# Optimization experiments

Hardware: AMD Instinct MI355X
Metric: run time of the kernel (lower is better)

Reference implementation:

```python
import jax, jax.numpy as jnp
import numpy as np
from jax import lax

D_MODEL = 512
N_STATE = 64
L = 1024
NC = 4  # n_components
HIDDEN = 2 * D_MODEL  # ChannelMix mult=2
R = D_MODEL // 8      # SE reduction
EPS = 1e-5


def hippo_A(N):
    n = np.arange(N, dtype=np.float32)
    t = 2.0 * n + 1.0
    sq = np.sqrt(t[:, None] * t[None, :])
    A = -np.tril(sq, -1) - np.diag(n + 1.0)
    return jnp.asarray(A, jnp.float32)


def setup_inputs() -> dict:
    key = jax.random.key(0)
    ks = jax.random.split(key, 12)
    d, N = D_MODEL, N_STATE
    n = np.arange(N, dtype=np.float32)
    Bref = jnp.asarray(np.sqrt(2.0 * n + 1.0), jnp.float32)
    Bp = jnp.tile(Bref[None, None, :], (NC, d, 1)) + 0.01 * jax.random.normal(ks[0], (NC, d, N))
    Cp = 0.1 * jax.random.normal(ks[1], (NC, d, N))
    Dp = jnp.zeros((NC, d))
    log_dt = jnp.log(0.1 * (1.5 ** jnp.arange(NC, dtype=jnp.float32)))
    x = jax.random.normal(ks[2], (8, L, d))
    s = 0.02
    return {
        "x": x,
        "Bp": Bp, "Cp": Cp, "Dp": Dp, "log_dt": log_dt,
        "se_w1": s * jax.random.normal(ks[3], (R, d)), "se_b1": jnp.zeros((R,)),
        "se_w2": s * jax.random.normal(ks[4], (d, R)), "se_b2": jnp.zeros((d,)),
        "n1_g": jnp.ones((d,)), "n1_b": jnp.zeros((d,)),
        "up_w": s * jax.random.normal(ks[5], (2 * HIDDEN, d)), "up_b": jnp.zeros((2 * HIDDEN,)),
        "down_w": s * jax.random.normal(ks[6], (d, HIDDEN)), "down_b": jnp.zeros((d,)),
        "mixn_g": jnp.ones((d,)), "mixn_b": jnp.zeros((d,)),
        "n2_g": jnp.ones((d,)), "n2_b": jnp.zeros((d,)),
    }


def _ln(x, g, b):
    m = jnp.mean(x, axis=-1, keepdims=True)
    v = jnp.mean(jnp.square(x - m), axis=-1, keepdims=True)
    return (x - m) * lax.rsqrt(v + EPS) * g + b


def _mixture_kernel(Bp, Cp, Dp, log_dt):
    A = hippo_A(N_STATE)
    I = jnp.eye(N_STATE, dtype=jnp.float32)

    def one(Bc, Cc, Dc, ldt):
        dt = jax.nn.softplus(ldt) + 1e-6
        lhs = I - 0.5 * dt * A
        rhs = I + 0.5 * dt * A
        A_bar = jnp.linalg.solve(lhs, rhs)          # (N,N)
        B_bar = jnp.linalg.solve(lhs, (dt * Bc).T).T  # (d,N)

        def step(xs, _):
            y = jnp.einsum('dn,dn->d', Cc, xs)
            return xs @ A_bar.T, y

        _, ys = lax.scan(step, B_bar, None, length=L)  # (L,d)
        K = ys.T  # (d,L)
        return K.at[:, 0].add(Dc)

    return jax.vmap(one)(Bp, Cp, Dp, log_dt).sum(0)  # (d,L)


def reference(x, Bp, Cp, Dp, log_dt,
              se_w1, se_b1, se_w2, se_b2,
              n1_g, n1_b, up_w, up_b, down_w, down_b,
              mixn_g, mixn_b, n2_g, n2_b):
    d = D_MODEL
    K = _mixture_kernel(Bp, Cp, Dp, log_dt)  # (d,L)

    # causal full-length depthwise conv1d
    x_dw = jnp.transpose(x, (0, 2, 1))  # (B,C,T)
    x_pad = jnp.pad(x_dw, ((0, 0), (0, 0), (L - 1, 0)))
    y = lax.conv_general_dilated(
        x_pad, K[:, None, :], window_strides=(1,), padding='VALID',
        feature_group_count=d, dimension_numbers=('NCH', 'OIH', 'NCH'))
    y = jnp.transpose(y, (0, 2, 1))  # (B,T,C)

    # SE gate (squeeze over time)
    s = jnp.mean(y, axis=1)  # (B,C)
    h = jax.nn.relu(s @ se_w1.T + se_b1)
    g = jax.nn.sigmoid(h @ se_w2.T + se_b2)
    y = y * g[:, None, :]

    y1 = _ln(x + y, n1_g, n1_b)

    # ChannelMix (GLU MLP) with residual + LN
    u = y1 @ up_w.T + up_b
    a, gg = jnp.split(u, 2, axis=-1)
    z = (jax.nn.gelu(a, approximate=False) * jax.nn.sigmoid(gg)) @ down_w.T + down_b
    z = _ln(y1 + z, mixn_g, mixn_b)

    return _ln(y1 + z, n2_g, n2_b)
```

## Files before the change

kernel.cpp:

```cpp
#include <hip/hip_runtime.h>
#include <math.h>


typedef short bf16x8 __attribute__((ext_vector_type(8)));
typedef float f32x4 __attribute__((ext_vector_type(4)));

__device__ __forceinline__ float fast_sigmoid(float x) { return 1.0f / (1.0f + __expf(-x)); }
__device__ __forceinline__ float fast_gelu(float x) {
    float u = 0.7978845608f * (x + 0.044715f * x * x * x);
    float t = 1.0f - 2.0f / (1.0f + __expf(2.0f * u));
    return 0.5f * x * (1.0f + t);
}
__device__ __forceinline__ unsigned short f2bf(float f) {
    unsigned u = __float_as_uint(f);
    unsigned r = (u + 0x7FFFu + ((u >> 16) & 1u)) >> 16;
    return (unsigned short)r;
}
__device__ __forceinline__ unsigned pk2(unsigned short a, unsigned short b) {
    return (unsigned)a | ((unsigned)b << 16);
}
__device__ __forceinline__ void gload16(const void* g, void* l) {
    __builtin_amdgcn_global_load_lds((const __attribute__((address_space(1))) unsigned int*)g,
                                     (__attribute__((address_space(3))) unsigned int*)l, 16, 0, 0);
}

__global__ __launch_bounds__(256) void front_kernel(const float* __restrict__ log_dt,
                                                    const float* __restrict__ Bp,
                                                    const float* __restrict__ up_w,
                                                    const float* __restrict__ dn_w,
                                                    const float* __restrict__ Cp,
                                                    const float* __restrict__ x,
                                                    float* __restrict__ Pow,
                                                    unsigned short* __restrict__ Bb_h,
                                                    unsigned short* __restrict__ Bb_l,
                                                    unsigned short* __restrict__ up_wb,
                                                    unsigned short* __restrict__ dn_wb,
                                                    unsigned short* __restrict__ Cp_h,
                                                    unsigned short* __restrict__ Cp_l,
                                                    float* __restrict__ xT) {
    __shared__ __align__(16) float smem[16640];
    int bid = blockIdx.x, tid = threadIdx.x;
    if (bid < 4) {
        float* M1 = smem;
        float* M1T = smem + 4096;
        float* M2 = smem + 8192;
        float* M2T = smem + 12288;
        int comp = bid;
        float ldt = log_dt[comp];
        float dt = log1pf(expf(ldt)) + 1e-6f;
        float hdt = 0.5f * dt;
        if (tid < 64) {
            int j = tid;
            float sqj = sqrtf(2.0f * (float)j + 1.0f);
            float S = 0.0f;
            for (int i = 0; i < 64; ++i) {
                float sqi = sqrtf(2.0f * (float)i + 1.0f);
                float r = (i == j) ? (1.0f - hdt * (float)(i + 1))
                                   : ((i > j) ? (-hdt * sqi * sqj) : 0.0f);
                float X = (r - hdt * sqi * S) / (1.0f + hdt * (float)(i + 1));
                M1[i * 64 + j] = X;
                M1T[j * 64 + i] = X;
                S += sqi * X;
            }
        }
        __syncthreads();
        for (int ii = tid; ii < 4096; ii += 256) Pow[(size_t)comp * 40960 + ii] = M1[ii];
        float* cur = M1; float* curT = M1T; float* nxt = M2; float* nxtT = M2T;
        int ti = tid >> 4, tj = tid & 15;
        for (int s = 1; s <= 9; ++s) {
            float c[4][4] = {{0}};
#pragma unroll 8
            for (int k = 0; k < 64; ++k) {
                float4 a = *(const float4*)&curT[k * 64 + ti * 4];
                float4 b = *(const float4*)&cur[k * 64 + tj * 4];
                c[0][0] += a.x * b.x; c[0][1] += a.x * b.y; c[0][2] += a.x * b.z; c[0][3] += a.x * b.w;
                c[1][0] += a.y * b.x; c[1][1] += a.y * b.y; c[1][2] += a.y * b.z; c[1][3] += a.y * b.w;
                c[2][0] += a.z * b.x; c[2][1] += a.z * b.y; c[2][2] += a.z * b.z; c[2][3] += a.z * b.w;
                c[3][0] += a.w * b.x; c[3][1] += a.w * b.y; c[3][2] += a.w * b.z; c[3][3] += a.w * b.w;
            }
#pragma unroll
            for (int r = 0; r < 4; ++r) {
                float4 row; row.x = c[r][0]; row.y = c[r][1]; row.z = c[r][2]; row.w = c[r][3];
                *(float4*)&nxt[(ti * 4 + r) * 64 + tj * 4] = row;
                float4 colv; colv.x = c[0][r]; colv.y = c[1][r]; colv.z = c[2][r]; colv.w = c[3][r];
                *(float4*)&nxtT[(tj * 4 + r) * 64 + ti * 4] = colv;
            }
            __syncthreads();
            for (int ii = tid; ii < 4096; ii += 256) Pow[(size_t)comp * 40960 + s * 4096 + ii] = nxt[ii];
            float* t0 = cur; cur = nxt; nxt = t0;
            float* t1 = curT; curT = nxtT; nxtT = t1;
            __syncthreads();
        }
    } else if (bid < 12) {
        int gid = (bid - 4) * 256 + tid;
        int comp = gid >> 9;
        float ldt = log_dt[comp];
        float dt = log1pf(expf(ldt)) + 1e-6f;
        float hdt = 0.5f * dt;
        const float* bp = Bp + (size_t)gid * 64;
        unsigned short* oh = Bb_h + (size_t)gid * 64;
        unsigned short* ol = Bb_l + (size_t)gid * 64;
        float S = 0.0f;
        for (int i = 0; i < 64; ++i) {
            float sqi = sqrtf(2.0f * (float)i + 1.0f);
            float y = (dt * bp[i] - hdt * sqi * S) / (1.0f + hdt * (float)(i + 1));
            unsigned short h = f2bf(y);
            oh[i] = h;
            ol[i] = f2bf(y - __uint_as_float((unsigned)h << 16));
            S += sqi * y;
        }
    } else if (bid < 844) {
        int i = (bid - 12) * 256 + tid;
        if (i < 196608) {
            const float* src = (i < 131072) ? up_w : dn_w;
            unsigned short* dst = (i < 131072) ? up_wb : dn_wb;
            int j = (i < 131072) ? i : (i - 131072);
            float4 a = ((const float4*)src)[2 * j];
            float4 b = ((const float4*)src)[2 * j + 1];
            uint4 o;
            o.x = pk2(f2bf(a.x), f2bf(a.y));
            o.y = pk2(f2bf(a.z), f2bf(a.w));
            o.z = pk2(f2bf(b.x), f2bf(b.y));
            o.w = pk2(f2bf(b.z), f2bf(b.w));
            *(uint4*)&dst[(size_t)j * 8] = o;
        } else if (i < 212992) {
            int j = i - 196608;
            float4 a = ((const float4*)Cp)[2 * j];
            float4 b = ((const float4*)Cp)[2 * j + 1];
            float vv[8] = {a.x, a.y, a.z, a.w, b.x, b.y, b.z, b.w};
            unsigned short hs[8], ls[8];
#pragma unroll
            for (int k = 0; k < 8; ++k) {
                unsigned short h = f2bf(vv[k]);
                hs[k] = h;
                ls[k] = f2bf(vv[k] - __uint_as_float((unsigned)h << 16));
            }
            uint4 ho, lo;
            ho.x = pk2(hs[0], hs[1]); ho.y = pk2(hs[2], hs[3]); ho.z = pk2(hs[4], hs[5]); ho.w = pk2(hs[6], hs[7]);
            lo.x = pk2(ls[0], ls[1]); lo.y = pk2(ls[2], ls[3]); lo.z = pk2(ls[4], ls[5]); lo.w = pk2(ls[6], ls[7]);
            *(uint4*)&Cp_h[(size_t)j * 8] = ho;
            *(uint4*)&Cp_l[(size_t)j * 8] = lo;
        }
    } else {
        int li = bid - 844;
        int bx = li & 31, by = (li >> 5) & 15, bz = li >> 9;
        float* tile = smem;
        int r0 = bx * 32, c0 = by * 32, b = bz;
        int tx = tid & 31, ty = tid >> 5;
#pragma unroll
        for (int m = 0; m < 4; ++m)
            tile[(ty + 8 * m) * 33 + tx] = x[((size_t)b * 1024 + r0 + ty + 8 * m) * 512 + c0 + tx];
        __syncthreads();
#pragma unroll
        for (int m = 0; m < 4; ++m)
            xT[((size_t)b * 512 + c0 + ty + 8 * m) * 1024 + r0 + tx] = tile[tx * 33 + ty + 8 * m];
    }
}

__global__ __launch_bounds__(256) void power_mats(const float* __restrict__ Pow,
                                                  unsigned short* __restrict__ Pst_h,
                                                  unsigned short* __restrict__ Pst_l,
                                                  unsigned short* __restrict__ Qst_h,
                                                  unsigned short* __restrict__ Qst_l) {
    int idx = blockIdx.x, comp = blockIdx.y, tid = threadIdx.x;
    __shared__ __align__(16) float R[4096], RT[4096], R2[4096], R2T[4096], SbT[4096];
    int isP = (idx < 32) ? 1 : 0;
    int f = isP ? idx : (idx - 32);
    int base_s = isP ? 0 : 5;
    const float* PowC = Pow + (size_t)comp * 40960;
    int i_ = tid & 63, kc = (tid >> 6) * 16;
    float* cur = R; float* curT = RT; float* nx = R2; float* nxT = R2T;
    if (f == 0) {
        for (int ii = tid; ii < 4096; ii += 256) {
            float v = ((ii >> 6) == (ii & 63)) ? 1.0f : 0.0f;
            R[ii] = v; RT[ii] = v;
        }
        __syncthreads();
    } else {
        int b0 = __ffs(f) - 1;
        const float* S0 = PowC + (size_t)(base_s + b0) * 4096;
#pragma unroll
        for (int j = 0; j < 16; j += 4) {
            float4 v = *(const float4*)&S0[i_ * 64 + kc + j];
            *(float4*)&R[i_ * 64 + kc + j] = v;
            RT[(kc + j + 0) * 64 + i_] = v.x;
            RT[(kc + j + 1) * 64 + i_] = v.y;
            RT[(kc + j + 2) * 64 + i_] = v.z;
            RT[(kc + j + 3) * 64 + i_] = v.w;
        }
        int rem = f & ~(1 << b0);
        int ti = tid >> 4, tj = tid & 15;
        __syncthreads();
        while (rem) {
            int b = __ffs(rem) - 1; rem &= rem - 1;
            const float* Sb = PowC + (size_t)(base_s + b) * 4096;
#pragma unroll
            for (int j = 0; j < 16; j += 4) {
                float4 v = *(const float4*)&Sb[i_ * 64 + kc + j];
                SbT[(kc + j + 0) * 64 + i_] = v.x;
                SbT[(kc + j + 1) * 64 + i_] = v.y;
                SbT[(kc + j + 2) * 64 + i_] = v.z;
                SbT[(kc + j + 3) * 64 + i_] = v.w;
            }
            __syncthreads();
            float c[4][4] = {{0}};
#pragma unroll 8
            for (int k = 0; k < 64; ++k) {
                float4 a = *(const float4*)&SbT[k * 64 + ti * 4];
                float4 b4 = *(const float4*)&cur[k * 64 + tj * 4];
                c[0][0] += a.x * b4.x; c[0][1] += a.x * b4.y; c[0][2] += a.x * b4.z; c[0][3] += a.x * b4.w;
                c[1][0] += a.y * b4.x; c[1][1] += a.y * b4.y; c[1][2] += a.y * b4.z; c[1][3] += a.y * b4.w;
                c[2][0] += a.z * b4.x; c[2][1] += a.z * b4.y; c[2][2] += a.z * b4.z; c[2][3] += a.z * b4.w;
                c[3][0] += a.w * b4.x; c[3][1] += a.w * b4.y; c[3][2] += a.w * b4.z; c[3][3] += a.w * b4.w;
            }
#pragma unroll
            for (int r = 0; r < 4; ++r) {
                float4 row; row.x = c[r][0]; row.y = c[r][1]; row.z = c[r][2]; row.w = c[r][3];
                *(float4*)&nx[(ti * 4 + r) * 64 + tj * 4] = row;
                float4 colv; colv.x = c[0][r]; colv.y = c[1][r]; colv.z = c[2][r]; colv.w = c[3][r];
                *(float4*)&nxT[(tj * 4 + r) * 64 + ti * 4] = colv;
            }
            __syncthreads();
            float* t0 = cur; cur = nx; nx = t0;
            float* t1 = curT; curT = nxT; nxT = t1;
        }
    }
    const float* src = isP ? cur : curT;
    int outrow = isP ? idx : (idx - 32);
    unsigned short* dh = (isP ? Pst_h : Qst_h) + (size_t)comp * 131072 + (size_t)outrow * 4096;
    unsigned short* dl = (isP ? Pst_l : Qst_l) + (size_t)comp * 131072 + (size_t)outrow * 4096;
    for (int ii = tid * 8; ii < 4096; ii += 2048) {
        float4 v0 = *(const float4*)&src[ii];
        float4 v1 = *(const float4*)&src[ii + 4];
        float vv[8] = {v0.x, v0.y, v0.z, v0.w, v1.x, v1.y, v1.z, v1.w};
        unsigned short hs[8], ls[8];
#pragma unroll
        for (int j = 0; j < 8; ++j) {
            unsigned short h = f2bf(vv[j]);
            hs[j] = h;
            ls[j] = f2bf(vv[j] - __uint_as_float((unsigned)h << 16));
        }
        uint4 ho, lo;
        ho.x = pk2(hs[0], hs[1]); ho.y = pk2(hs[2], hs[3]); ho.z = pk2(hs[4], hs[5]); ho.w = pk2(hs[6], hs[7]);
        lo.x = pk2(ls[0], ls[1]); lo.y = pk2(ls[2], ls[3]); lo.z = pk2(ls[4], ls[5]); lo.w = pk2(ls[6], ls[7]);
        *(uint4*)&dh[ii] = ho;
        *(uint4*)&dl[ii] = lo;
    }
}

__global__ __launch_bounds__(256) void kgemm_uv2(const unsigned short* __restrict__ Bb_h,
                                                 const unsigned short* __restrict__ Bb_l,
                                                 const unsigned short* __restrict__ Pst_h,
                                                 const unsigned short* __restrict__ Pst_l,
                                                 const unsigned short* __restrict__ Cp_h,
                                                 const unsigned short* __restrict__ Cp_l,
                                                 const unsigned short* __restrict__ Qst_h,
                                                 const unsigned short* __restrict__ Qst_l,
                                                 unsigned short* __restrict__ V_h,
                                                 unsigned short* __restrict__ V_l,
                                                 unsigned short* __restrict__ U_h,
                                                 unsigned short* __restrict__ U_l) {
    int zz = blockIdx.z;
    int isV = (zz < 4) ? 1 : 0;
    int comp = isV ? zz : (zz - 4);
    const unsigned short* Ah = isV ? Bb_h : Cp_h;
    const unsigned short* Al = isV ? Bb_l : Cp_l;
    const unsigned short* Bh = isV ? Pst_h : Qst_h;
    const unsigned short* Bl = isV ? Pst_l : Qst_l;
    unsigned short* Ch = isV ? V_h : U_h;
    unsigned short* Cl = isV ? V_l : U_l;
    int m0 = blockIdx.x * 128, n0 = blockIdx.y * 64;
    int tid = threadIdx.x, w = tid >> 6, l = tid & 63;
    __shared__ __align__(16) short Ash[8192], Asl[8192], Bsh[4096], Bsl[4096];
    const unsigned short* Abh = Ah + (size_t)comp * 32768;
    const unsigned short* Abl = Al + (size_t)comp * 32768;
    const unsigned short* Bbh = Bh + (size_t)comp * 131072;
    const unsigned short* Bbl = Bl + (size_t)comp * 131072;
#pragma unroll
    for (int i = 0; i < 4; ++i) {
        int cid = tid + 256 * i;
        int row = cid >> 3, slot = cid & 7;
        int goff = (m0 + row) * 64 + slot * 8;
        int loff = row * 64 + (slot ^ (row & 7)) * 8;
        *(uint4*)&Ash[loff] = *(const uint4*)(Abh + goff);
        *(uint4*)&Asl[loff] = *(const uint4*)(Abl + goff);
    }
#pragma unroll
    for (int i = 0; i < 2; ++i) {
        int cid = tid + 256 * i;
        int row = cid >> 3, slot = cid & 7;
        int goff = (n0 + row) * 64 + slot * 8;
        int loff = row * 64 + (slot ^ (row & 7)) * 8;
        *(uint4*)&Bsh[loff] = *(const uint4*)(Bbh + goff);
        *(uint4*)&Bsl[loff] = *(const uint4*)(Bbl + goff);
    }
    __syncthreads();
    int p = l >> 4, lr = l & 15;
    f32x4 acc[2][4];
#pragma unroll
    for (int rt = 0; rt < 2; ++rt)
#pragma unroll
        for (int ct = 0; ct < 4; ++ct) acc[rt][ct] = (f32x4)0.0f;
#pragma unroll
    for (int ks = 0; ks < 2; ++ks) {
        bf16x8 ah2[2], al2[2], bh2[4], bl2[4];
#pragma unroll
        for (int rt = 0; rt < 2; ++rt) {
            int row = w * 32 + rt * 16 + lr;
            int off = row * 64 + ((ks * 4 + p) ^ (row & 7)) * 8;
            ah2[rt] = *(bf16x8*)&Ash[off];
            al2[rt] = *(bf16x8*)&Asl[off];
        }
#pragma unroll
        for (int ct = 0; ct < 4; ++ct) {
            int cr = ct * 16 + lr;
            int off = cr * 64 + ((ks * 4 + p) ^ (cr & 7)) * 8;
            bh2[ct] = *(bf16x8*)&Bsh[off];
            bl2[ct] = *(bf16x8*)&Bsl[off];
        }
#pragma unroll
        for (int rt = 0; rt < 2; ++rt)
#pragma unroll
            for (int ct = 0; ct < 4; ++ct) {
                acc[rt][ct] = __builtin_amdgcn_mfma_f32_16x16x32_bf16(ah2[rt], bh2[ct], acc[rt][ct], 0, 0, 0);
                acc[rt][ct] = __builtin_amdgcn_mfma_f32_16x16x32_bf16(ah2[rt], bl2[ct], acc[rt][ct], 0, 0, 0);
                acc[rt][ct] = __builtin_amdgcn_mfma_f32_16x16x32_bf16(al2[rt], bh2[ct], acc[rt][ct], 0, 0, 0);
            }
    }
#pragma unroll
    for (int rt = 0; rt < 2; ++rt)
#pragma unroll
        for (int ct = 0; ct < 4; ++ct) {
#pragma unroll
            for (int reg = 0; reg < 4; ++reg) {
                int row = m0 + w * 32 + rt * 16 + p * 4 + reg;
                int col = n0 + ct * 16 + lr;
                float v = acc[rt][ct][reg];
                unsigned short h = f2bf(v);
                unsigned short lo2 = f2bf(v - __uint_as_float((unsigned)h << 16));
                size_t o = (size_t)comp * 1048576 + (size_t)row * 2048 + col;
                Ch[o] = h;
                Cl[o] = lo2;
            }
        }
}

__global__ __launch_bounds__(256) void kgemm_kr(const unsigned short* __restrict__ Uh,
                                                const unsigned short* __restrict__ Ul,
                                                const unsigned short* __restrict__ Vh,
                                                const unsigned short* __restrict__ Vl,
                                                const float* __restrict__ Dp,
                                                float* __restrict__ Kr) {
    int tid = threadIdx.x, w = tid >> 6, l = tid & 63;
    int d = blockIdx.x;
    int g = w * 512 + d;
    int p = l >> 4, lr = l & 15;
    __shared__ float ksh[4096];
    const unsigned short* ubh = Uh + (size_t)g * 2048;
    const unsigned short* ubl = Ul + (size_t)g * 2048;
    const unsigned short* vbh = Vh + (size_t)g * 2048;
    const unsigned short* vbl = Vl + (size_t)g * 2048;
    f32x4 acc[2][2];
    acc[0][0] = (f32x4)0.0f; acc[0][1] = (f32x4)0.0f;
    acc[1][0] = (f32x4)0.0f; acc[1][1] = (f32x4)0.0f;
#pragma unroll
    for (int ks = 0; ks < 2; ++ks) {
        bf16x8 uh2[2], ul2[2], vh2[2], vl2[2];
#pragma unroll
        for (int mt = 0; mt < 2; ++mt) {
            int off = (mt * 16 + lr) * 64 + ks * 32 + p * 8;
            uh2[mt] = *(const bf16x8*)(ubh + off);
            ul2[mt] = *(const bf16x8*)(ubl + off);
            vh2[mt] = *(const bf16x8*)(vbh + off);
            vl2[mt] = *(const bf16x8*)(vbl + off);
        }
#pragma unroll
        for (int mt = 0; mt < 2; ++mt)
#pragma unroll
            for (int nt = 0; nt < 2; ++nt) {
                acc[mt][nt] = __builtin_amdgcn_mfma_f32_16x16x32_bf16(uh2[mt], vh2[nt], acc[mt][nt], 0, 0, 0);
                acc[mt][nt] = __builtin_amdgcn_mfma_f32_16x16x32_bf16(uh2[mt], vl2[nt], acc[mt][nt], 0, 0, 0);
                acc[mt][nt] = __builtin_amdgcn_mfma_f32_16x16x32_bf16(ul2[mt], vh2[nt], acc[mt][nt], 0, 0, 0);
            }
    }
#pragma unroll
    for (int mt = 0; mt < 2; ++mt)
#pragma unroll
        for (int nt = 0; nt < 2; ++nt)
#pragma unroll
            for (int reg = 0; reg < 4; ++reg) {
                int q = mt * 16 + p * 4 + reg;
                int r = nt * 16 + lr;
                ksh[w * 1024 + q * 32 + r] = acc[mt][nt][reg];
            }
    __syncthreads();
#pragma unroll
    for (int j = 0; j < 4; ++j) {
        int ll = tid * 4 + j;
        float s = ksh[ll] + ksh[1024 + ll] + ksh[2048 + ll] + ksh[3072 + ll];
        if (ll == 0) s += Dp[d] + Dp[512 + d] + Dp[1024 + d] + Dp[1536 + d];
        Kr[(size_t)d * 1024 + (1023 - ll)] = s;
    }
}

__global__ __launch_bounds__(256) void conv_mfma(const float* __restrict__ xT,
                                                 const float* __restrict__ Kr,
                                                 float* __restrict__ yT,
                                                 float* __restrict__ ssum) {
    int c = blockIdx.x, tid = threadIdx.x;
    int w = tid >> 6, l = tid & 63;
    __shared__ __align__(16) float krp[1088];
    __shared__ __align__(16) short xh[8512], xl[8512];
    __shared__ __align__(16) short gh[10240], gl[10240];
    __shared__ float ssh[64];

    {
        float4 kv = *(const float4*)&Kr[(size_t)c * 1024 + tid * 4];
        *(float4*)&krp[32 + tid * 4] = kv;
        if (tid < 8) *(float4*)&krp[tid * 4] = make_float4(0, 0, 0, 0);
        else if (tid < 16) *(float4*)&krp[1056 + (tid - 8) * 4] = make_float4(0, 0, 0, 0);
    }
    if (tid < 32) {
        int b = tid >> 2, g = tid & 3;
        uint4 z = {0, 0, 0, 0};
        *(uint4*)&xh[(b * 133 + g) * 8] = z;
    } else if (tid < 64) {
        int t2 = tid - 32; int b = t2 >> 2, g = t2 & 3;
        uint4 z = {0, 0, 0, 0};
        *(uint4*)&xl[(b * 133 + g) * 8] = z;
    }
#pragma unroll
    for (int i = 0; i < 4; ++i) {
        int gid = tid + 256 * i;
        int b = gid >> 7, gt = gid & 127;
        const float* src = &xT[((size_t)(b * 512 + c)) * 1024 + gt * 8];
        float4 v0 = *(const float4*)src;
        float4 v1 = *(const float4*)(src + 4);
        float vv[8] = {v0.x, v0.y, v0.z, v0.w, v1.x, v1.y, v1.z, v1.w};
        unsigned short hsv[8], lsv[8];
#pragma unroll
        for (int j2 = 0; j2 < 8; ++j2) {
            unsigned short h = f2bf(vv[j2]);
            hsv[j2] = h;
            lsv[j2] = f2bf(vv[j2] - __uint_as_float((unsigned)h << 16));
        }
        uint4 hh, ll;
        hh.x = pk2(hsv[0], hsv[1]); hh.y = pk2(hsv[2], hsv[3]);
        hh.z = pk2(hsv[4], hsv[5]); hh.w = pk2(hsv[6], hsv[7]);
        ll.x = pk2(lsv[0], lsv[1]); ll.y = pk2(lsv[2], lsv[3]);
        ll.z = pk2(lsv[4], lsv[5]); ll.w = pk2(lsv[6], lsv[7]);
        int off = (b * 133 + 4 + gt) * 8;
        *(uint4*)&xh[off] = hh;
        *(uint4*)&xl[off] = ll;
    }
    __syncthreads();

    f32x4 acc[4][2];
#pragma unroll
    for (int i = 0; i < 4; ++i) { acc[i][0] = (f32x4)0.0f; acc[i][1] = (f32x4)0.0f; }

    int lr = l & 15, kg4 = l >> 4;
    for (int ch = 0; ch < 4; ++ch) {
        int dq0 = ch * 8;
        {
            int dqloc = tid >> 5, n = tid & 31, dq = dq0 + dqloc;
            int s0 = 32 * dq + n + 1;
            int a0 = s0 & ~3, sh = s0 & 3;
            float ff[36];
#pragma unroll
            for (int i = 0; i < 9; ++i) *(float4*)&ff[i * 4] = *(const float4*)&krp[a0 + i * 4];
            unsigned short hsv[32], lsv[32];
#pragma unroll
            for (int k = 0; k < 32; ++k) {
                int j2 = 31 - k;
                float v = (sh == 0) ? ff[j2] : (sh == 1) ? ff[j2 + 1] : (sh == 2) ? ff[j2 + 2] : ff[j2 + 3];
                unsigned short h = f2bf(v);
                hsv[k] = h;
                lsv[k] = f2bf(v - __uint_as_float((unsigned)h << 16));
            }
            int gbase = (dqloc * 32 + n) * 5 * 8;
#pragma unroll
            for (int kg = 0; kg < 4; ++kg) {
                uint4 hh, ll;
                hh.x = pk2(hsv[8 * kg + 0], hsv[8 * kg + 1]);
                hh.y = pk2(hsv[8 * kg + 2], hsv[8 * kg + 3]);
                hh.z = pk2(hsv[8 * kg + 4], hsv[8 * kg + 5]);
                hh.w = pk2(hsv[8 * kg + 6], hsv[8 * kg + 7]);
                ll.x = pk2(lsv[8 * kg + 0], lsv[8 * kg + 1]);
                ll.y = pk2(lsv[8 * kg + 2], lsv[8 * kg + 3]);
                ll.z = pk2(lsv[8 * kg + 4], lsv[8 * kg + 5]);
                ll.w = pk2(lsv[8 * kg + 6], lsv[8 * kg + 7]);
                *(uint4*)&gh[gbase + kg * 8] = hh;
                *(uint4*)&gl[gbase + kg * 8] = ll;
            }
        }
        __syncthreads();
        for (int dqloc = 0; dqloc < 8; ++dqloc) {
            int dq = dq0 + dqloc;
            bf16x8 bh[2], bl[2];
#pragma unroll
            for (int nf = 0; nf < 2; ++nf) {
                int go = ((dqloc * 32 + nf * 16 + lr) * 5 + kg4) * 8;
                bh[nf] = *(bf16x8*)&gh[go];
                bl[nf] = *(bf16x8*)&gl[go];
            }
#pragma unroll
            for (int ffi = 0; ffi < 4; ++ffi) {
                int F = w + 4 * ffi;
                if (2 * F + 1 < dq) continue;
                int b = lr & 7, qoff = lr >> 3;
                int q = 2 * F + qoff;
                int j = 4 * (q - dq) + kg4 + 4;
                int xo = (b * 133 + j) * 8;
                bf16x8 ah = *(bf16x8*)&xh[xo];
                bf16x8 al = *(bf16x8*)&xl[xo];
#pragma unroll
                for (int nf = 0; nf < 2; ++nf) {
                    acc[ffi][nf] = __builtin_amdgcn_mfma_f32_16x16x32_bf16(ah, bh[nf], acc[ffi][nf], 0, 0, 0);
                    acc[ffi][nf] = __builtin_amdgcn_mfma_f32_16x16x32_bf16(al, bh[nf], acc[ffi][nf], 0, 0, 0);
                    acc[ffi][nf] = __builtin_amdgcn_mfma_f32_16x16x32_bf16(ah, bl[nf], acc[ffi][nf], 0, 0, 0);
                }
            }
        }
        __syncthreads();
    }

    float bsum[4] = {0, 0, 0, 0};
#pragma unroll
    for (int ffi = 0; ffi < 4; ++ffi) {
        int F = w + 4 * ffi;
#pragma unroll
        for (int nf = 0; nf < 2; ++nf) {
#pragma unroll
            for (int reg = 0; reg < 4; ++reg) {
                int mloc = 4 * kg4 + reg;
                int b = mloc & 7;
                int q = 2 * F + (mloc >> 3);
                int t = 32 * q + nf * 16 + lr;
                yT[((size_t)(b * 512 + c)) * 1024 + t] = acc[ffi][nf][reg];
                bsum[reg] += acc[ffi][nf][reg];
            }
        }
    }
#pragma unroll
    for (int off = 1; off < 16; off <<= 1) {
#pragma unroll
        for (int reg = 0; reg < 4; ++reg) bsum[reg] += __shfl_xor(bsum[reg], off, 64);
    }
    if (lr == 0) {
#pragma unroll
        for (int reg = 0; reg < 4; ++reg) ssh[w * 16 + kg4 * 4 + reg] = bsum[reg];
    }
    __syncthreads();
    if (tid < 8) {
        float tot = 0.0f;
        for (int w2 = 0; w2 < 4; ++w2) tot += ssh[w2 * 16 + tid] + ssh[w2 * 16 + 8 + tid];
        ssum[tid * 512 + c] = tot;
    }
}

__global__ __launch_bounds__(256) void se_kernel(const float* __restrict__ ssum,
                                                 const float* __restrict__ w1,
                                                 const float* __restrict__ b1,
                                                 const float* __restrict__ w2,
                                                 const float* __restrict__ b2,
                                                 float* __restrict__ g) {
    int b = blockIdx.x, tid = threadIdx.x;
    __shared__ float s_sh[512];
    __shared__ float part[256];
    __shared__ float h_sh[64];
    for (int c = tid; c < 512; c += 256) s_sh[c] = ssum[b * 512 + c] * (1.0f / 1024.0f);
    __syncthreads();
    int r = tid & 63, seg = tid >> 6;
    float p = 0.0f;
    for (int c = seg * 128; c < seg * 128 + 128; ++c) p += s_sh[c] * w1[r * 512 + c];
    part[tid] = p;
    __syncthreads();
    if (tid < 64) {
        float h = part[tid] + part[tid + 64] + part[tid + 128] + part[tid + 192] + b1[tid];
        h_sh[tid] = fmaxf(h, 0.0f);
    }
    __syncthreads();
    for (int c = tid; c < 512; c += 256) {
        float acc = b2[c];
#pragma unroll 8
        for (int rr = 0; rr < 64; ++rr) acc += h_sh[rr] * w2[c * 64 + rr];
        g[b * 512 + c] = 1.0f / (1.0f + expf(-acc));
    }
}

__global__ __launch_bounds__(256) void fuse1t(const float* __restrict__ x,
                                              const float* __restrict__ yT,
                                              const float* __restrict__ g,
                                              const float* __restrict__ n1g,
                                              const float* __restrict__ n1b,
                                              unsigned short* __restrict__ y1b) {
    int ti = blockIdx.x, b = blockIdx.y, t0 = ti * 16, tid = threadIdx.x;
    __shared__ float tile[512 * 17];
    __shared__ float red1[256], red2[256];
    for (int i = tid; i < 2048; i += 256) {
        int c = i >> 2, tq = (i & 3) * 4;
        float4 v = *(const float4*)&yT[((size_t)(b * 512 + c)) * 1024 + t0 + tq];
        tile[c * 17 + tq + 0] = v.x;
        tile[c * 17 + tq + 1] = v.y;
        tile[c * 17 + tq + 2] = v.z;
        tile[c * 17 + tq + 3] = v.w;
    }
    __syncthreads();
    int tloc = tid >> 4, cg = tid & 15;
    int t = t0 + tloc;
    float vbuf[32];
    float s1 = 0.0f, s2 = 0.0f;
#pragma unroll
    for (int m = 0; m < 8; ++m) {
        int c = cg * 4 + 64 * m;
        float4 xv = *(const float4*)&x[((size_t)(b * 1024 + t)) * 512 + c];
        float4 gv = *(const float4*)&g[b * 512 + c];
        float v0 = xv.x + tile[(c + 0) * 17 + tloc] * gv.x;
        float v1 = xv.y + tile[(c + 1) * 17 + tloc] * gv.y;
        float v2 = xv.z + tile[(c + 2) * 17 + tloc] * gv.z;
        float v3 = xv.w + tile[(c + 3) * 17 + tloc] * gv.w;
        vbuf[m * 4 + 0] = v0; vbuf[m * 4 + 1] = v1;
        vbuf[m * 4 + 2] = v2; vbuf[m * 4 + 3] = v3;
        s1 += v0 + v1 + v2 + v3;
        s2 += v0 * v0 + v1 * v1 + v2 * v2 + v3 * v3;
    }
    red1[tid] = s1; red2[tid] = s2;
    __syncthreads();
    if (cg == 0) {
        float a1 = 0.0f, a2 = 0.0f;
#pragma unroll
        for (int k = 0; k < 16; ++k) { a1 += red1[tloc * 16 + k]; a2 += red2[tloc * 16 + k]; }
        red1[tloc * 16] = a1; red2[tloc * 16] = a2;
    }
    __syncthreads();
    float mean = red1[tloc * 16] * (1.0f / 512.0f);
    float var = red2[tloc * 16] * (1.0f / 512.0f) - mean * mean;
    float rstd = rsqrtf(var + 1e-5f);
#pragma unroll
    for (int m = 0; m < 8; ++m) {
        int c = cg * 4 + 64 * m;
        float4 g4 = *(const float4*)&n1g[c];
        float4 b4 = *(const float4*)&n1b[c];
        float o0 = (vbuf[m * 4 + 0] - mean) * rstd * g4.x + b4.x;
        float o1 = (vbuf[m * 4 + 1] - mean) * rstd * g4.y + b4.y;
        float o2 = (vbuf[m * 4 + 2] - mean) * rstd * g4.z + b4.z;
        float o3 = (vbuf[m * 4 + 3] - mean) * rstd * g4.w + b4.w;
        uint2 pk;
        pk.x = pk2(f2bf(o0), f2bf(o1));
        pk.y = pk2(f2bf(o2), f2bf(o3));
        *(uint2*)&y1b[((size_t)(b * 1024 + t)) * 512 + c] = pk;
    }
}

__device__ __forceinline__ int swz8(int slot, int row) { return slot ^ (row & 7); }

__global__ __launch_bounds__(256) void gemm_glu(const unsigned short* __restrict__ A,
                                                const unsigned short* __restrict__ W,
                                                const float* __restrict__ bias,
                                                unsigned short* __restrict__ act) {
    const int K = 512;
    int id = blockIdx.x;
    int xcd = id & 7, local = id >> 3;
    int bx = 16 * xcd + (local & 15);
    int by = local >> 4;
    int m0 = bx * 64, n0 = by * 64;
    int tid = threadIdx.x, w = tid >> 6, l = tid & 63;
    __shared__ __align__(16) short As[2][4096];
    __shared__ __align__(16) short Bs[2][8192];
    const unsigned short* gA[2];
#pragma unroll
    for (int i = 0; i < 2; ++i) {
        int s = 2 * w + i;
        int row = 8 * s + (l >> 3);
        gA[i] = A + (size_t)(m0 + row) * K + (size_t)(((l & 7) ^ (row & 7)) * 8);
    }
    const unsigned short* gB[4];
#pragma unroll
    for (int i = 0; i < 4; ++i) {
        int s = 4 * w + i;
        int rb = 8 * s + (l >> 3);
        int grow = (rb < 64) ? (n0 + rb) : (1024 + n0 + rb - 64);
        gB[i] = W + (size_t)grow * K + (size_t)(((l & 7) ^ (rb & 7)) * 8);
    }
    int p = l >> 4, lr = l & 15;
    int arow = w * 16 + lr;
    f32x4 accA[4], accG[4];
#pragma unroll
    for (int ct = 0; ct < 4; ++ct) { accA[ct] = (f32x4)0.0f; accG[ct] = (f32x4)0.0f; }
#pragma unroll
    for (int i = 0; i < 2; ++i) gload16(gA[i], &As[0][(2 * w + i) * 512]);
#pragma unroll
    for (int i = 0; i < 4; ++i) gload16(gB[i], &Bs[0][(4 * w + i) * 512]);
    int cur = 0;
    for (int kt = 0; kt < K; kt += 64) {
        __syncthreads();
        if (kt + 64 < K) {
            int nb = cur ^ 1;
#pragma unroll
            for (int i = 0; i < 2; ++i) gload16(gA[i] + kt + 64, &As[nb][(2 * w + i) * 512]);
#pragma unroll
            for (int i = 0; i < 4; ++i) gload16(gB[i] + kt + 64, &Bs[nb][(4 * w + i) * 512]);
        }
#pragma unroll
        for (int ks = 0; ks < 2; ++ks) {
            int slot = ks * 4 + p;
            bf16x8 af = *(bf16x8*)&As[cur][arow * 64 + swz8(slot, arow) * 8];
            bf16x8 bA[4], bG[4];
#pragma unroll
            for (int ct = 0; ct < 4; ++ct) {
                int ca = ct * 16 + lr, cg = 64 + ct * 16 + lr;
                bA[ct] = *(bf16x8*)&Bs[cur][ca * 64 + swz8(slot, ca) * 8];
                bG[ct] = *(bf16x8*)&Bs[cur][cg * 64 + swz8(slot, cg) * 8];
            }
#pragma unroll
            for (int ct = 0; ct < 4; ++ct) {
                accA[ct] = __builtin_amdgcn_mfma_f32_16x16x32_bf16(af, bA[ct], accA[ct], 0, 0, 0);
                accG[ct] = __builtin_amdgcn_mfma_f32_16x16x32_bf16(af, bG[ct], accG[ct], 0, 0, 0);
            }
        }
        cur ^= 1;
    }
#pragma unroll
    for (int ct = 0; ct < 4; ++ct) {
        int col = n0 + ct * 16 + lr;
        float ba = bias[col], bg = bias[1024 + col];
#pragma unroll
        for (int reg = 0; reg < 4; ++reg) {
            int row = m0 + w * 16 + p * 4 + reg;
            float a = accA[ct][reg] + ba;
            float gg = accG[ct][reg] + bg;
            act[(size_t)row * 1024 + col] = f2bf(fast_gelu(a) * fast_sigmoid(gg));
        }
    }
}

__global__ __launch_bounds__(256) void gemm_plain(const unsigned short* __restrict__ A,
                                                  const unsigned short* __restrict__ W,
                                                  const float* __restrict__ bias,
                                                  float* __restrict__ Cout) {
    const int K = 1024, N = 512;
    int id = blockIdx.x;
    int xcd = id & 7, local = id >> 3;
    int bx = 16 * xcd + (local & 15);
    int by = local >> 4;
    int m0 = bx * 64, n0 = by * 64;
    int tid = threadIdx.x, w = tid >> 6, l = tid & 63;
    int wr = w >> 1, wc = w & 1;
    __shared__ __align__(16) short As[2][4096];
    __shared__ __align__(16) short Bs[2][4096];
    const unsigned short* gA[2];
    const unsigned short* gB[2];
#pragma unroll
    for (int i = 0; i < 2; ++i) {
        int s = 2 * w + i;
        int row = 8 * s + (l >> 3);
        int koff = ((l & 7) ^ (row & 7)) * 8;
        gA[i] = A + (size_t)(m0 + row) * K + koff;
        gB[i] = W + (size_t)(n0 + row) * K + koff;
    }
    int p = l >> 4, lr = l & 15;
    f32x4 acc[2][2];
#pragma unroll
    for (int i = 0; i < 2; ++i)
#pragma unroll
        for (int j = 0; j < 2; ++j) acc[i][j] = (f32x4)0.0f;
#pragma unroll
    for (int i = 0; i < 2; ++i) {
        gload16(gA[i], &As[0][(2 * w + i) * 512]);
        gload16(gB[i], &Bs[0][(2 * w + i) * 512]);
    }
    int cur = 0;
    for (int kt = 0; kt < K; kt += 64) {
        __syncthreads();
        if (kt + 64 < K) {
            int nb = cur ^ 1;
#pragma unroll
            for (int i = 0; i < 2; ++i) {
                gload16(gA[i] + kt + 64, &As[nb][(2 * w + i) * 512]);
                gload16(gB[i] + kt + 64, &Bs[nb][(2 * w + i) * 512]);
            }
        }
#pragma unroll
        for (int ks = 0; ks < 2; ++ks) {
            int slot = ks * 4 + p;
            bf16x8 af[2], bfr[2];
#pragma unroll
            for (int t = 0; t < 2; ++t) {
                int r = wr * 32 + t * 16 + lr;
                af[t] = *(bf16x8*)&As[cur][r * 64 + swz8(slot, r) * 8];
                int cq = wc * 32 + t * 16 + lr;
                bfr[t] = *(bf16x8*)&Bs[cur][cq * 64 + swz8(slot, cq) * 8];
            }
#pragma unroll
            for (int i = 0; i < 2; ++i)
#pragma unroll
                for (int j = 0; j < 2; ++j)
                    acc[i][j] = __builtin_amdgcn_mfma_f32_16x16x32_bf16(af[i], bfr[j], acc[i][j], 0, 0, 0);
        }
        cur ^= 1;
    }
#pragma unroll
    for (int i = 0; i < 2; ++i)
#pragma unroll
        for (int j = 0; j < 2; ++j) {
            int col = n0 + wc * 32 + j * 16 + lr;
            float bb = bias[col];
#pragma unroll
            for (int reg = 0; reg < 4; ++reg) {
                int row = m0 + wr * 32 + i * 16 + p * 4 + reg;
                Cout[(size_t)row * N + col] = acc[i][j][reg] + bb;
            }
        }
}

__global__ __launch_bounds__(128) void fuse2_kernel(const unsigned short* __restrict__ y1b,
                                                    const float* __restrict__ z,
                                                    const float* __restrict__ mg,
                                                    const float* __restrict__ mb,
                                                    const float* __restrict__ g2,
                                                    const float* __restrict__ b2v,
                                                    float* __restrict__ out) {
    int row = blockIdx.x, tid = threadIdx.x, c = tid * 4;
    __shared__ float r1[2], r2[2];
    uint2 yu = *(const uint2*)&y1b[(size_t)row * 512 + c];
    float4 a;
    a.x = __uint_as_float(yu.x << 16);
    a.y = __uint_as_float(yu.x & 0xffff0000u);
    a.z = __uint_as_float(yu.y << 16);
    a.w = __uint_as_float(yu.y & 0xffff0000u);
    float4 zv = *(const float4*)&z[(size_t)row * 512 + c];
    float4 t1;
    t1.x = a.x + zv.x; t1.y = a.y + zv.y; t1.z = a.z + zv.z; t1.w = a.w + zv.w;
    float s1 = t1.x + t1.y + t1.z + t1.w;
    float s2 = t1.x * t1.x + t1.y * t1.y + t1.z * t1.z + t1.w * t1.w;
#pragma unroll
    for (int off = 32; off > 0; off >>= 1) {
        s1 += __shfl_down(s1, off, 64);
        s2 += __shfl_down(s2, off, 64);
    }
    if ((tid & 63) == 0) { r1[tid >> 6] = s1; r2[tid >> 6] = s2; }
    __syncthreads();
    float mean = (r1[0] + r1[1]) * (1.0f / 512.0f);
    float var = (r2[0] + r2[1]) * (1.0f / 512.0f) - mean * mean;
    float rstd = rsqrtf(var + 1e-5f);
    float4 mg4 = *(const float4*)&mg[c];
    float4 mb4 = *(const float4*)&mb[c];
    float4 t2;
    t2.x = a.x + ((t1.x - mean) * rstd * mg4.x + mb4.x);
    t2.y = a.y + ((t1.y - mean) * rstd * mg4.y + mb4.y);
    t2.z = a.z + ((t1.z - mean) * rstd * mg4.z + mb4.z);
    t2.w = a.w + ((t1.w - mean) * rstd * mg4.w + mb4.w);
    __syncthreads();
    s1 = t2.x + t2.y + t2.z + t2.w;
    s2 = t2.x * t2.x + t2.y * t2.y + t2.z * t2.z + t2.w * t2.w;
#pragma unroll
    for (int off = 32; off > 0; off >>= 1) {
        s1 += __shfl_down(s1, off, 64);
        s2 += __shfl_down(s2, off, 64);
    }
    if ((tid & 63) == 0) { r1[tid >> 6] = s1; r2[tid >> 6] = s2; }
    __syncthreads();
    float mean2 = (r1[0] + r1[1]) * (1.0f / 512.0f);
    float var2 = (r2[0] + r2[1]) * (1.0f / 512.0f) - mean2 * mean2;
    float rstd2 = rsqrtf(var2 + 1e-5f);
    float4 gg = *(const float4*)&g2[c];
    float4 bb = *(const float4*)&b2v[c];
    float4 o;
    o.x = (t2.x - mean2) * rstd2 * gg.x + bb.x;
    o.y = (t2.y - mean2) * rstd2 * gg.y + bb.y;
    o.z = (t2.z - mean2) * rstd2 * gg.z + bb.z;
    o.w = (t2.w - mean2) * rstd2 * gg.w + bb.w;
    *(float4*)&out[(size_t)row * 512 + c] = o;
}

extern "C" void kernel_launch(void* const* d_in, const int* in_sizes, int n_in,
                              void* d_out, int out_size, void* d_ws, size_t ws_size,
                              hipStream_t stream) {
    (void)in_sizes; (void)n_in; (void)out_size; (void)ws_size;
    const float* x      = (const float*)d_in[0];
    const float* Bp     = (const float*)d_in[1];
    const float* Cp     = (const float*)d_in[2];
    const float* Dp     = (const float*)d_in[3];
    const float* log_dt = (const float*)d_in[4];
    const float* se_w1  = (const float*)d_in[5];
    const float* se_b1  = (const float*)d_in[6];
    const float* se_w2  = (const float*)d_in[7];
    const float* se_b2  = (const float*)d_in[8];
    const float* n1g    = (const float*)d_in[9];
    const float* n1b    = (const float*)d_in[10];
    const float* up_w   = (const float*)d_in[11];
    const float* up_b   = (const float*)d_in[12];
    const float* dn_w   = (const float*)d_in[13];
    const float* dn_b   = (const float*)d_in[14];
    const float* mxg    = (const float*)d_in[15];
    const float* mxb    = (const float*)d_in[16];
    const float* n2g    = (const float*)d_in[17];
    const float* n2b    = (const float*)d_in[18];

    float* ws = (float*)d_ws;
    float* Kr   = ws + 0;
    float* ssum = ws + 524352;
    float* gbuf = ws + 528448;
    unsigned short* up_wb = (unsigned short*)(ws + 532544);
    unsigned short* dn_wb = (unsigned short*)(ws + 1056832);
    float* Pow  = ws + 1450048;
    unsigned short* Bb_h = (unsigned short*)(ws + 1613888);
    unsigned short* Bb_l = (unsigned short*)(ws + 1679424);
    unsigned short* Cp_h = (unsigned short*)(ws + 1744960);
    unsigned short* Cp_l = (unsigned short*)(ws + 1810496);
    unsigned short* Pst_h = (unsigned short*)(ws + 1876032);
    unsigned short* Pst_l = (unsigned short*)(ws + 2138176);
    unsigned short* Qst_h = (unsigned short*)(ws + 2400320);
    unsigned short* Qst_l = (unsigned short*)(ws + 2662464);
    unsigned short* U_h = (unsigned short*)(ws + 5021760);
    unsigned short* U_l = (unsigned short*)(ws + 7118912);
    unsigned short* V_h = (unsigned short*)(ws + 9216064);
    unsigned short* V_l = (unsigned short*)(ws + 11313216);
    float* xT   = ws + 5021760;
    float* yT   = ws + 9216064;
    float* zb   = ws + 13410368;
    unsigned short* act = (unsigned short*)(ws + 5021760);
    unsigned short* y1b = (unsigned short*)(ws + 20971520);
    float* outp = (float*)d_out;

    unsigned short* U_h2 = (unsigned short*)(ws + 25165824);
    unsigned short* U_l2 = (unsigned short*)(ws + 27262976);
    unsigned short* V_h2 = (unsigned short*)(ws + 29360128);
    unsigned short* V_l2 = (unsigned short*)(ws + 31457280);
    (void)U_h; (void)U_l; (void)V_h; (void)V_l; (void)yT;
    float* yT2 = ws + 9216064;

    hipLaunchKernelGGL(front_kernel, dim3(4940), dim3(256), 0, stream,
                       log_dt, Bp, up_w, dn_w, Cp, x,
                       Pow, Bb_h, Bb_l, up_wb, dn_wb, Cp_h, Cp_l, xT);
    hipLaunchKernelGGL(power_mats, dim3(64, 4), dim3(256), 0, stream, Pow, Pst_h, Pst_l, Qst_h, Qst_l);
    hipLaunchKernelGGL(kgemm_uv2, dim3(4, 32, 8), dim3(256), 0, stream,
                       Bb_h, Bb_l, Pst_h, Pst_l, Cp_h, Cp_l, Qst_h, Qst_l, V_h2, V_l2, U_h2, U_l2);
    hipLaunchKernelGGL(kgemm_kr, dim3(512), dim3(256), 0, stream, U_h2, U_l2, V_h2, V_l2, Dp, Kr);
    hipLaunchKernelGGL(conv_mfma, dim3(512), dim3(256), 0, stream, xT, Kr, yT2, ssum);
    hipLaunchKernelGGL(se_kernel, dim3(8), dim3(256), 0, stream, ssum, se_w1, se_b1, se_w2, se_b2, gbuf);
    hipLaunchKernelGGL(fuse1t, dim3(64, 8), dim3(256), 0, stream, x, yT2, gbuf, n1g, n1b, y1b);
    hipLaunchKernelGGL(gemm_glu, dim3(2048), dim3(256), 0, stream, y1b, up_wb, up_b, act);
    hipLaunchKernelGGL(gemm_plain, dim3(1024), dim3(256), 0, stream, act, dn_wb, dn_b, zb);
    hipLaunchKernelGGL(fuse2_kernel, dim3(8192), dim3(128), 0, stream, y1b, zb, mxg, mxb, n2g, n2b, outp);
}
```

Measured before the change: 204.6 us.

## Replace LDS-staged GEMMs with direct-global MFMA loads and larger per-wave tiles

Both MLP GEMMs (GLU up-projection and down-projection) drop the LDS double-buffered staging and the __syncthreads. Each wave now loads its MFMA fragments straight from global memory, and each block covers a 128-row tile with 32 rows per wave, which halves the grid sizes. The aim is to remove barrier and LDS traffic and raise per-wave register reuse. The cost is that operands are no longer shared through LDS: each wave independently re-reads the same weight columns from global memory/L2, and the 16-byte-per-lane row-strided loads may coalesce poorly.

```diff
diff --git a/kernel.cpp b/kernel.cpp
--- a/kernel.cpp
+++ b/kernel.cpp
@@ -18,10 +18,6 @@
 }
 __device__ __forceinline__ unsigned pk2(unsigned short a, unsigned short b) {
     return (unsigned)a | ((unsigned)b << 16);
-}
-__device__ __forceinline__ void gload16(const void* g, void* l) {
-    __builtin_amdgcn_global_load_lds((const __attribute__((address_space(1))) unsigned int*)g,
-                                     (__attribute__((address_space(3))) unsigned int*)l, 16, 0, 0);
 }
 
 __global__ __launch_bounds__(256) void front_kernel(const float* __restrict__ log_dt,
@@ -653,8 +649,6 @@
     }
 }
 
-__device__ __forceinline__ int swz8(int slot, int row) { return slot ^ (row & 7); }
-
 __global__ __launch_bounds__(256) void gemm_glu(const unsigned short* __restrict__ A,
                                                 const unsigned short* __restrict__ W,
                                                 const float* __restrict__ bias,
@@ -662,77 +656,63 @@
     const int K = 512;
     int id = blockIdx.x;
     int xcd = id & 7, local = id >> 3;
-    int bx = 16 * xcd + (local & 15);
-    int by = local >> 4;
-    int m0 = bx * 64, n0 = by * 64;
-    int tid = threadIdx.x, w = tid >> 6, l = tid & 63;
-    __shared__ __align__(16) short As[2][4096];
-    __shared__ __align__(16) short Bs[2][8192];
-    const unsigned short* gA[2];
-#pragma unroll
-    for (int i = 0; i < 2; ++i) {
-        int s = 2 * w + i;
-        int row = 8 * s + (l >> 3);
-        gA[i] = A + (size_t)(m0 + row) * K + (size_t)(((l & 7) ^ (row & 7)) * 8);
-    }
-    const unsigned short* gB[4];
-#pragma unroll
-    for (int i = 0; i < 4; ++i) {
-        int s = 4 * w + i;
-        int rb = 8 * s + (l >> 3);
-        int grow = (rb < 64) ? (n0 + rb) : (1024 + n0 + rb - 64);
-        gB[i] = W + (size_t)grow * K + (size_t)(((l & 7) ^ (rb & 7)) * 8);
-    }
+    int mg = 8 * xcd + (local & 7);
+    int nt = local >> 3;
+    int w = threadIdx.x >> 6, l = threadIdx.x & 63;
+    int m0 = mg * 128 + w * 32;
+    int n0 = nt * 64;
     int p = l >> 4, lr = l & 15;
-    int arow = w * 16 + lr;
-    f32x4 accA[4], accG[4];
-#pragma unroll
-    for (int ct = 0; ct < 4; ++ct) { accA[ct] = (f32x4)0.0f; accG[ct] = (f32x4)0.0f; }
-#pragma unroll
-    for (int i = 0; i < 2; ++i) gload16(gA[i], &As[0][(2 * w + i) * 512]);
-#pragma unroll
-    for (int i = 0; i < 4; ++i) gload16(gB[i], &Bs[0][(4 * w + i) * 512]);
-    int cur = 0;
-    for (int kt = 0; kt < K; kt += 64) {
-        __syncthreads();
-        if (kt + 64 < K) {
-            int nb = cur ^ 1;
-#pragma unroll
-            for (int i = 0; i < 2; ++i) gload16(gA[i] + kt + 64, &As[nb][(2 * w + i) * 512]);
-#pragma unroll
-            for (int i = 0; i < 4; ++i) gload16(gB[i] + kt + 64, &Bs[nb][(4 * w + i) * 512]);
-        }
-#pragma unroll
-        for (int ks = 0; ks < 2; ++ks) {
-            int slot = ks * 4 + p;
-            bf16x8 af = *(bf16x8*)&As[cur][arow * 64 + swz8(slot, arow) * 8];
-            bf16x8 bA[4], bG[4];
+    const unsigned short* pA[2];
+#pragma unroll
+    for (int rt = 0; rt < 2; ++rt)
+        pA[rt] = A + (size_t)(m0 + rt * 16 + lr) * K + 8 * p;
+    const unsigned short* pB[8];
+#pragma unroll
+    for (int ct = 0; ct < 4; ++ct) {
+        pB[ct] = W + (size_t)(n0 + ct * 16 + lr) * K + 8 * p;
+        pB[4 + ct] = W + (size_t)(1024 + n0 + ct * 16 + lr) * K + 8 * p;
+    }
+    f32x4 accA[2][4], accG[2][4];
+#pragma unroll
+    for (int rt = 0; rt < 2; ++rt)
+#pragma unroll
+        for (int ct = 0; ct < 4; ++ct) {
+            accA[rt][ct] = (f32x4)0.0f;
+            accG[rt][ct] = (f32x4)0.0f;
+        }
+#pragma unroll 4
+    for (int kt = 0; kt < K; kt += 32) {
+        bf16x8 af[2];
+#pragma unroll
+        for (int rt = 0; rt < 2; ++rt) af[rt] = *(const bf16x8*)(pA[rt] + kt);
+        bf16x8 bA[4], bG[4];
+#pragma unroll
+        for (int ct = 0; ct < 4; ++ct) {
+            bA[ct] = *(const bf16x8*)(pB[ct] + kt);
+            bG[ct] = *(const bf16x8*)(pB[4 + ct] + kt);
+        }
+#pragma unroll
+        for (int rt = 0; rt < 2; ++rt)
 #pragma unroll
             for (int ct = 0; ct < 4; ++ct) {
-                int ca = ct * 16 + lr, cg = 64 + ct * 16 + lr;
-                bA[ct] = *(bf16x8*)&Bs[cur][ca * 64 + swz8(slot, ca) * 8];
-                bG[ct] = *(bf16x8*)&Bs[cur][cg * 64 + swz8(slot, cg) * 8];
-            }
-#pragma unroll
-            for (int ct = 0; ct < 4; ++ct) {
-                accA[ct] = __builtin_amdgcn_mfma_f32_16x16x32_bf16(af, bA[ct], accA[ct], 0, 0, 0);
-                accG[ct] = __builtin_amdgcn_mfma_f32_16x16x32_bf16(af, bG[ct], accG[ct], 0, 0, 0);
-            }
-        }
-        cur ^= 1;
-    }
-#pragma unroll
-    for (int ct = 0; ct < 4; ++ct) {
-        int col = n0 + ct * 16 + lr;
-        float ba = bias[col], bg = bias[1024 + col];
-#pragma unroll
-        for (int reg = 0; reg < 4; ++reg) {
-            int row = m0 + w * 16 + p * 4 + reg;
-            float a = accA[ct][reg] + ba;
-            float gg = accG[ct][reg] + bg;
-            act[(size_t)row * 1024 + col] = f2bf(fast_gelu(a) * fast_sigmoid(gg));
-        }
-    }
+                accA[rt][ct] = __builtin_amdgcn_mfma_f32_16x16x32_bf16(af[rt], bA[ct], accA[rt][ct], 0, 0, 0);
+                accG[rt][ct] = __builtin_amdgcn_mfma_f32_16x16x32_bf16(af[rt], bG[ct], accG[rt][ct], 0, 0, 0);
+            }
+    }
+#pragma unroll
+    for (int rt = 0; rt < 2; ++rt)
+#pragma unroll
+        for (int ct = 0; ct < 4; ++ct) {
+            int col = n0 + ct * 16 + lr;
+            float ba = bias[col], bg = bias[1024 + col];
+#pragma unroll
+            for (int reg = 0; reg < 4; ++reg) {
+                int row = m0 + rt * 16 + p * 4 + reg;
+                float a = accA[rt][ct][reg] + ba;
+                float gg = accG[rt][ct][reg] + bg;
+                act[(size_t)row * 1024 + col] = f2bf(fast_gelu(a) * fast_sigmoid(gg));
+            }
+        }
 }
 
 __global__ __launch_bounds__(256) void gemm_plain(const unsigned short* __restrict__ A,
@@ -742,74 +722,49 @@
     const int K = 1024, N = 512;
     int id = blockIdx.x;
     int xcd = id & 7, local = id >> 3;
-    int bx = 16 * xcd + (local & 15);
-    int by = local >> 4;
-    int m0 = bx * 64, n0 = by * 64;
-    int tid = threadIdx.x, w = tid >> 6, l = tid & 63;
-    int wr = w >> 1, wc = w & 1;
-    __shared__ __align__(16) short As[2][4096];
-    __shared__ __align__(16) short Bs[2][4096];
-    const unsigned short* gA[2];
-    const unsigned short* gB[2];
-#pragma unroll
-    for (int i = 0; i < 2; ++i) {
-        int s = 2 * w + i;
-        int row = 8 * s + (l >> 3);
-        int koff = ((l & 7) ^ (row & 7)) * 8;
-        gA[i] = A + (size_t)(m0 + row) * K + koff;
-        gB[i] = W + (size_t)(n0 + row) * K + koff;
-    }
+    int mg = 8 * xcd + (local & 7);
+    int nt = local >> 3;
+    int w = threadIdx.x >> 6, l = threadIdx.x & 63;
+    int m0 = mg * 128 + w * 32;
+    int n0 = nt * 64;
     int p = l >> 4, lr = l & 15;
-    f32x4 acc[2][2];
-#pragma unroll
-    for (int i = 0; i < 2; ++i)
-#pragma unroll
-        for (int j = 0; j < 2; ++j) acc[i][j] = (f32x4)0.0f;
-#pragma unroll
-    for (int i = 0; i < 2; ++i) {
-        gload16(gA[i], &As[0][(2 * w + i) * 512]);
-        gload16(gB[i], &Bs[0][(2 * w + i) * 512]);
-    }
-    int cur = 0;
-    for (int kt = 0; kt < K; kt += 64) {
-        __syncthreads();
-        if (kt + 64 < K) {
-            int nb = cur ^ 1;
-#pragma unroll
-            for (int i = 0; i < 2; ++i) {
-                gload16(gA[i] + kt + 64, &As[nb][(2 * w + i) * 512]);
-                gload16(gB[i] + kt + 64, &Bs[nb][(2 * w + i) * 512]);
-            }
-        }
-#pragma unroll
-        for (int ks = 0; ks < 2; ++ks) {
-            int slot = ks * 4 + p;
-            bf16x8 af[2], bfr[2];
-#pragma unroll
-            for (int t = 0; t < 2; ++t) {
-                int r = wr * 32 + t * 16 + lr;
-                af[t] = *(bf16x8*)&As[cur][r * 64 + swz8(slot, r) * 8];
-                int cq = wc * 32 + t * 16 + lr;
-                bfr[t] = *(bf16x8*)&Bs[cur][cq * 64 + swz8(slot, cq) * 8];
-            }
-#pragma unroll
-            for (int i = 0; i < 2; ++i)
-#pragma unroll
-                for (int j = 0; j < 2; ++j)
-                    acc[i][j] = __builtin_amdgcn_mfma_f32_16x16x32_bf16(af[i], bfr[j], acc[i][j], 0, 0, 0);
-        }
-        cur ^= 1;
-    }
-#pragma unroll
-    for (int i = 0; i < 2; ++i)
-#pragma unroll
-        for (int j = 0; j < 2; ++j) {
-            int col = n0 + wc * 32 + j * 16 + lr;
+    const unsigned short* pA[2];
+#pragma unroll
+    for (int rt = 0; rt < 2; ++rt)
+        pA[rt] = A + (size_t)(m0 + rt * 16 + lr) * K + 8 * p;
+    const unsigned short* pB[4];
+#pragma unroll
+    for (int ct = 0; ct < 4; ++ct)
+        pB[ct] = W + (size_t)(n0 + ct * 16 + lr) * K + 8 * p;
+    f32x4 acc[2][4];
+#pragma unroll
+    for (int rt = 0; rt < 2; ++rt)
+#pragma unroll
+        for (int ct = 0; ct < 4; ++ct) acc[rt][ct] = (f32x4)0.0f;
+#pragma unroll 4
+    for (int kt = 0; kt < K; kt += 32) {
+        bf16x8 af[2];
+#pragma unroll
+        for (int rt = 0; rt < 2; ++rt) af[rt] = *(const bf16x8*)(pA[rt] + kt);
+        bf16x8 bfr[4];
+#pragma unroll
+        for (int ct = 0; ct < 4; ++ct) bfr[ct] = *(const bf16x8*)(pB[ct] + kt);
+#pragma unroll
+        for (int rt = 0; rt < 2; ++rt)
+#pragma unroll
+            for (int ct = 0; ct < 4; ++ct)
+                acc[rt][ct] = __builtin_amdgcn_mfma_f32_16x16x32_bf16(af[rt], bfr[ct], acc[rt][ct], 0, 0, 0);
+    }
+#pragma unroll
+    for (int rt = 0; rt < 2; ++rt)
+#pragma unroll
+        for (int ct = 0; ct < 4; ++ct) {
+            int col = n0 + ct * 16 + lr;
             float bb = bias[col];
 #pragma unroll
             for (int reg = 0; reg < 4; ++reg) {
-                int row = m0 + wr * 32 + i * 16 + p * 4 + reg;
-                Cout[(size_t)row * N + col] = acc[i][j][reg] + bb;
+                int row = m0 + rt * 16 + p * 4 + reg;
+                Cout[(size_t)row * N + col] = acc[rt][ct][reg] + bb;
             }
         }
 }
@@ -913,23 +868,16 @@
     unsigned short* Pst_l = (unsigned short*)(ws + 2138176);
     unsigned short* Qst_h = (unsigned short*)(ws + 2400320);
     unsigned short* Qst_l = (unsigned short*)(ws + 2662464);
-    unsigned short* U_h = (unsigned short*)(ws + 5021760);
-    unsigned short* U_l = (unsigned short*)(ws + 7118912);
-    unsigned short* V_h = (unsigned short*)(ws + 9216064);
-    unsigned short* V_l = (unsigned short*)(ws + 11313216);
     float* xT   = ws + 5021760;
-    float* yT   = ws + 9216064;
+    float* yT2  = ws + 9216064;
     float* zb   = ws + 13410368;
     unsigned short* act = (unsigned short*)(ws + 5021760);
     unsigned short* y1b = (unsigned short*)(ws + 20971520);
-    float* outp = (float*)d_out;
-
     unsigned short* U_h2 = (unsigned short*)(ws + 25165824);
     unsigned short* U_l2 = (unsigned short*)(ws + 27262976);
     unsigned short* V_h2 = (unsigned short*)(ws + 29360128);
     unsigned short* V_l2 = (unsigned short*)(ws + 31457280);
-    (void)U_h; (void)U_l; (void)V_h; (void)V_l; (void)yT;
-    float* yT2 = ws + 9216064;
+    float* outp = (float*)d_out;
 
     hipLaunchKernelGGL(front_kernel, dim3(4940), dim3(256), 0, stream,
                        log_dt, Bp, up_w, dn_w, Cp, x,
@@ -941,7 +889,7 @@
     hipLaunchKernelGGL(conv_mfma, dim3(512), dim3(256), 0, stream, xT, Kr, yT2, ssum);
     hipLaunchKernelGGL(se_kernel, dim3(8), dim3(256), 0, stream, ssum, se_w1, se_b1, se_w2, se_b2, gbuf);
     hipLaunchKernelGGL(fuse1t, dim3(64, 8), dim3(256), 0, stream, x, yT2, gbuf, n1g, n1b, y1b);
-    hipLaunchKernelGGL(gemm_glu, dim3(2048), dim3(256), 0, stream, y1b, up_wb, up_b, act);
-    hipLaunchKernelGGL(gemm_plain, dim3(1024), dim3(256), 0, stream, act, dn_wb, dn_b, zb);
+    hipLaunchKernelGGL(gemm_glu, dim3(1024), dim3(256), 0, stream, y1b, up_wb, up_b, act);
+    hipLaunchKernelGGL(gemm_plain, dim3(512), dim3(256), 0, stream, act, dn_wb, dn_b, zb);
     hipLaunchKernelGGL(fuse2_kernel, dim3(8192), dim3(128), 0, stream, y1b, zb, mxg, mxb, n2g, n2b, outp);
 }
```

Result: slower. 271.6 us (+32.8%).
